# Performance work log

Measured on AMD Instinct MI355X. Metric: run time of the kernel, lower is better.

The kernel has to match this reference:

```python
import jax, jax.numpy as jnp
import numpy as np

NUM_HIDDENS = 512
NUM_HEADS = 4
B, S = 4, 2048


def setup_inputs() -> dict:
    key = jax.random.key(0)
    ks = jax.random.split(key, 10)
    H = NUM_HIDDENS
    scale = 1.0 / np.sqrt(H)
    return {
        "queries": jax.random.normal(ks[0], (B, S, H), jnp.float32),
        "keys": jax.random.normal(ks[1], (B, S, H), jnp.float32),
        "values": jax.random.normal(ks[2], (B, S, H), jnp.float32),
        "attention_mask": jax.random.randint(ks[3], (B, S), 0, 2).astype(bool),
        "Wq": jax.random.normal(ks[4], (H, H), jnp.float32) * scale,
        "bq": jnp.zeros((H,), jnp.float32),
        "Wk": jax.random.normal(ks[5], (H, H), jnp.float32) * scale,
        "bk": jnp.zeros((H,), jnp.float32),
        "Wv": jax.random.normal(ks[6], (H, H), jnp.float32) * scale,
        "bv": jnp.zeros((H,), jnp.float32),
    }


def reference(queries, keys, values, attention_mask, Wq, bq, Wk, bk, Wv, bv):
    B_, S_, H = queries.shape
    nh = NUM_HEADS
    dh = H // nh

    # QKV projections with ReLU (as in the original Sequential(Linear, ReLU))
    q = jax.nn.relu(jnp.einsum("bsh,oh->bso", queries, Wq) + bq)
    k = jax.nn.relu(jnp.einsum("bsh,oh->bso", keys, Wk) + bk)
    v = jax.nn.relu(jnp.einsum("bsh,oh->bso", values, Wv) + bv)

    # chunk along last dim + stack dim=1  ==  reshape [B,S,nh,dh] -> [B,nh,S,dh]
    qs = q.reshape(B_, S_, nh, dh).transpose(0, 2, 1, 3)
    ks_ = k.reshape(B_, S_, nh, dh).transpose(0, 2, 1, 3)
    vs = v.reshape(B_, S_, nh, dh).transpose(0, 2, 1, 3)

    # scores [B, nh, S, S]
    score = jnp.einsum("bhqd,bhkd->bhqk", qs, ks_) / jnp.sqrt(jnp.float32(dh))

    # 'enc' mask: [B,S] -> [B,1,S,1], fills entire QUERY rows (faithful quirk)
    row_mask = attention_mask[:, None, :, None]
    score = jnp.where(row_mask, jnp.float32(-1e9), score)

    attn = jax.nn.softmax(score, axis=-1)
    a = jnp.einsum("bhqk,bhkd->bhqd", attn, vs)  # [B, nh, S, dh]

    # faithful quirk: permute(0,1,3,2) then reshape to (B, S, H)
    a = jnp.transpose(a, (0, 1, 3, 2)).reshape(B_, S_, H)
    return a + queries
```

## Files before the change

### kernel.cpp

```cpp
#include <hip/hip_runtime.h>
#include <hip/hip_bf16.h>

typedef __attribute__((ext_vector_type(8)))  __bf16 bf16x8;
typedef __attribute__((ext_vector_type(4)))  __bf16 bf16x4;
typedef __attribute__((ext_vector_type(2)))  __bf16 bf16x2;
typedef __attribute__((ext_vector_type(4)))  float  f32x4;
typedef __attribute__((ext_vector_type(16))) float  f32x16;

#define MFMA16(a,b,c) __builtin_amdgcn_mfma_f32_16x16x32_bf16((a),(b),(c),0,0,0)
#define MFMA32(a,b,c) __builtin_amdgcn_mfma_f32_32x32x16_bf16((a),(b),(c),0,0,0)

__device__ inline void gload_lds16(const __bf16* g, __bf16* l) {
  __builtin_amdgcn_global_load_lds(
      (const __attribute__((address_space(1))) void*)g,
      (__attribute__((address_space(3))) void*)l, 16, 0, 0);
}

__global__ __launch_bounds__(256) void proj_kernel(
    const float* __restrict__ Xq, const float* __restrict__ Xk,
    const float* __restrict__ Xv, const float* __restrict__ Wq,
    const float* __restrict__ Wk, const float* __restrict__ Wv,
    const float* __restrict__ bq, const float* __restrict__ bk,
    const float* __restrict__ bv, __bf16* __restrict__ dq,
    __bf16* __restrict__ dk, __bf16* __restrict__ dv)
{
  const int which = blockIdx.z;
  const float* X   = which == 0 ? Xq : which == 1 ? Xk : Xv;
  const float* W   = which == 0 ? Wq : which == 1 ? Wk : Wv;
  const float* bias= which == 0 ? bq : which == 1 ? bk : bv;
  __bf16* dst      = which == 0 ? dq : which == 1 ? dk : dv;
  const float oscale = which == 0 ? 0.12751744710339033f : 1.0f;
  const int mode = (which == 2);

  __shared__ __bf16 Al[64][72];
  __shared__ __bf16 Wl[64][72];
  const int tid  = threadIdx.x;
  const int lane = tid & 63;
  const int w    = tid >> 6;
  const int wr = w >> 1, wc = w & 1;
  const int mbase = blockIdx.x * 64;
  const int nbase = blockIdx.y * 64;
  const int arow = lane & 15;
  const int kgrp = (lane >> 4) * 8;
  f32x4 acc[2][2] = {};

  for (int k0 = 0; k0 < 512; k0 += 64) {
    __syncthreads();
#pragma unroll
    for (int i = 0; i < 4; ++i) {
      int idx = tid + i * 256;
      int r = idx >> 4, c = (idx & 15) * 4;
      float4 a  = *(const float4*)&X[(size_t)(mbase + r) * 512 + k0 + c];
      float4 bb = *(const float4*)&W[(size_t)(nbase + r) * 512 + k0 + c];
      bf16x4 av, bv2;
      av[0] = (__bf16)a.x;  av[1] = (__bf16)a.y;  av[2] = (__bf16)a.z;  av[3] = (__bf16)a.w;
      bv2[0] = (__bf16)bb.x; bv2[1] = (__bf16)bb.y; bv2[2] = (__bf16)bb.z; bv2[3] = (__bf16)bb.w;
      *(bf16x4*)&Al[r][c] = av;
      *(bf16x4*)&Wl[r][c] = bv2;
    }
    __syncthreads();
#pragma unroll
    for (int kk = 0; kk < 2; ++kk) {
      bf16x8 af[2], bfr[2];
      const int kcol = kk * 32 + kgrp;
#pragma unroll
      for (int m = 0; m < 2; ++m)
        af[m] = *(bf16x8*)&Al[wr * 32 + m * 16 + arow][kcol];
#pragma unroll
      for (int n = 0; n < 2; ++n)
        bfr[n] = *(bf16x8*)&Wl[wc * 32 + n * 16 + arow][kcol];
#pragma unroll
      for (int m = 0; m < 2; ++m)
#pragma unroll
        for (int n = 0; n < 2; ++n)
          acc[m][n] = MFMA16(af[m], bfr[n], acc[m][n]);
    }
  }

#pragma unroll
  for (int m = 0; m < 2; ++m) {
#pragma unroll
    for (int n = 0; n < 2; ++n) {
      int col  = nbase + wc * 32 + n * 16 + (lane & 15);
      int row0 = mbase + wr * 32 + m * 16 + ((lane >> 4) << 2);
      float bsv = bias[col];
      int h = col >> 7, d = col & 127;
#pragma unroll
      for (int r = 0; r < 4; ++r) {
        float v = acc[m][n][r] + bsv;
        v = (v > 0.0f ? v : 0.0f) * oscale;
        int mm = row0 + r;
        int b = mm >> 11, s = mm & 2047;
        if (mode == 0)
          dst[((size_t)(b * 4 + h) * 2048 + s) * 128 + d] = (__bf16)v;
        else
          dst[((size_t)(b * 4 + h) * 128 + d) * 2048 + s] = (__bf16)v;
      }
    }
  }
}

__global__ __launch_bounds__(256, 2) void attn_kernel(
    const __bf16* __restrict__ qh, const __bf16* __restrict__ kh,
    const __bf16* __restrict__ vt, const int* __restrict__ mask,
    const float* __restrict__ queries, float* __restrict__ out)
{
  __shared__ __align__(16) __bf16 Kl[2][64 * 128];
  __shared__ __align__(16) __bf16 Vl[2][128 * 64];

  const int tid  = threadIdx.x;
  const int lane = tid & 63;
  const int w    = tid >> 6;
  const int qw   = w & 1;
  const int kw   = w >> 1;
  const int r5   = lane & 31;
  const int hi32 = lane >> 5;

  const int blk = blockIdx.x;
  const int xcd = blk & 7;
  const int idx = blk >> 3;
  const int bh  = xcd * 2 + (idx & 1);
  const int qt  = idx >> 1;
  const int b = bh >> 2, h = bh & 3;
  const int qbase = qt * 64 + qw * 32;

  const __bf16* qptr = qh + (size_t)bh * 2048 * 128;
  const __bf16* kptr = kh + (size_t)bh * 2048 * 128;
  const __bf16* vptr = vt + (size_t)bh * 128 * 2048;

  bf16x8 qf[8];
#pragma unroll
  for (int ds = 0; ds < 8; ++ds)
    qf[ds] = *(const bf16x8*)&qptr[(size_t)(qbase + r5) * 128 + ds * 16 + hi32 * 8];

  const bool mrow = mask[b * 2048 + qbase + r5] != 0;

  float m_st = -1e30f, l_st = 0.f;
  f32x16 oacc[4] = {};

  auto stageK = [&](int buf, int kv0) {
#pragma unroll
    for (int i = 0; i < 4; ++i) {
      int ob = i * 4096 + w * 1024;
      int o  = ob + lane * 16;
      int r  = o >> 8;
      int s  = ((o >> 4) & 15) ^ (r & 7);
      gload_lds16(kptr + (size_t)(kv0 + r) * 128 + s * 8, &Kl[buf][ob >> 1]);
    }
  };
  auto stageV = [&](int buf, int kv0) {
#pragma unroll
    for (int i = 0; i < 4; ++i) {
      int ob = i * 4096 + w * 1024;
      int o  = ob + lane * 16;
      int r  = o >> 7;
      int s  = ((o >> 4) & 7) ^ (r & 7);
      gload_lds16(vptr + (size_t)r * 2048 + kv0 + s * 8, &Vl[buf][ob >> 1]);
    }
  };

  stageK(0, 0);
  stageV(0, 0);

  for (int t = 0; t < 32; ++t) {
    const int cur = t & 1;
    if (t < 31) {
      stageK(cur ^ 1, (t + 1) * 64);
      stageV(cur ^ 1, (t + 1) * 64);
      asm volatile("s_waitcnt vmcnt(8)" ::: "memory");
    } else {
      asm volatile("s_waitcnt vmcnt(0)" ::: "memory");
    }
    __builtin_amdgcn_s_barrier();

    f32x16 sacc = {};
    __builtin_amdgcn_s_setprio(1);
#pragma unroll
    for (int ds = 0; ds < 8; ++ds) {
      int row = kw * 32 + r5;
      int sl  = ((ds * 2 + hi32) ^ (row & 7)) * 8;
      bf16x8 kf = *(bf16x8*)&Kl[cur][row * 128 + sl];
      sacc = MFMA32(kf, qf[ds], sacc);
    }
    __builtin_amdgcn_s_setprio(0);

#pragma unroll
    for (int r = 0; r < 16; ++r)
      sacc[r] = mrow ? -1e9f : sacc[r];

    float pmax = sacc[0];
#pragma unroll
    for (int r = 1; r < 16; ++r) pmax = fmaxf(pmax, sacc[r]);
    pmax = fmaxf(pmax, __shfl_xor(pmax, 32));

    if (!__all(pmax - m_st <= 8.0f)) {
      float mn = fmaxf(m_st, pmax);
      float rs = __builtin_amdgcn_exp2f(m_st - mn);
      m_st = mn;
      l_st *= rs;
#pragma unroll
      for (int dblk = 0; dblk < 4; ++dblk)
#pragma unroll
        for (int r = 0; r < 16; ++r)
          oacc[dblk][r] *= rs;
    }

    float rsum = 0.f;
#pragma unroll
    for (int r = 0; r < 16; ++r) {
      float p = __builtin_amdgcn_exp2f(sacc[r] - m_st);
      sacc[r] = p;
      rsum += p;
    }
    rsum += __shfl_xor(rsum, 32);
    l_st += rsum;

    unsigned pk[8];
#pragma unroll
    for (int g = 0; g < 8; ++g) {
      bf16x2 tp;
      tp[0] = (__bf16)sacc[2 * g];
      tp[1] = (__bf16)sacc[2 * g + 1];
      pk[g] = __builtin_bit_cast(unsigned, tp);
    }
    bf16x8 pf[2];
#pragma unroll
    for (int s = 0; s < 2; ++s) {
      unsigned a0 = pk[4 * s + 0], a1 = pk[4 * s + 1];
      unsigned b0 = pk[4 * s + 2], b1 = pk[4 * s + 3];
      asm("v_permlane32_swap_b32 %0, %1" : "+v"(a0), "+v"(b0));
      asm("v_permlane32_swap_b32 %0, %1" : "+v"(a1), "+v"(b1));
      union { unsigned u[4]; bf16x8 v; } pu;
      pu.u[0] = a0; pu.u[1] = a1; pu.u[2] = b0; pu.u[3] = b1;
      pf[s] = pu.v;
    }

    __builtin_amdgcn_s_setprio(1);
#pragma unroll
    for (int dblk = 0; dblk < 4; ++dblk) {
#pragma unroll
      for (int s = 0; s < 2; ++s) {
        int row = dblk * 32 + r5;
        int s0  = kw * 4 + s * 2 + hi32;
        int sl  = (s0 ^ (row & 7)) * 8;
        bf16x8 vf = *(bf16x8*)&Vl[cur][row * 64 + sl];
        oacc[dblk] = MFMA32(vf, pf[s], oacc[dblk]);
      }
    }
    __builtin_amdgcn_s_setprio(0);

    __builtin_amdgcn_s_barrier();
  }

  __syncthreads();
  float* Ml = (float*)&Kl[0][0];
  float* Ll = Ml + 64;
  float* Ob = Ml + 128;

  if (kw == 1) {
    if (hi32 == 0) { Ml[qw * 32 + r5] = m_st; Ll[qw * 32 + r5] = l_st; }
    float* dst = Ob + (size_t)(qw * 64 + lane) * 68;
#pragma unroll
    for (int dblk = 0; dblk < 4; ++dblk)
      *(f32x16*)(dst + dblk * 16) = oacc[dblk];
  }
  __syncthreads();

  if (kw == 0) {
    float m1 = Ml[qw * 32 + r5], l1 = Ll[qw * 32 + r5];
    float mm = fmaxf(m_st, m1);
    float w0 = __builtin_amdgcn_exp2f(m_st - mm);
    float w1 = __builtin_amdgcn_exp2f(m1 - mm);
    float inv = 1.0f / (l_st * w0 + l1 * w1);
    const float* src = Ob + (size_t)(qw * 64 + lane) * 68;

    const int qhi = qt >> 3;
    const int col = (qt & 7) * 64 + qw * 32 + r5;
#pragma unroll
    for (int dblk = 0; dblk < 4; ++dblk) {
      f32x16 o1 = *(const f32x16*)(src + dblk * 16);
#pragma unroll
      for (int r = 0; r < 16; ++r) {
        int d = dblk * 32 + (r & 3) + 8 * (r >> 2) + 4 * hi32;
        int srow = h * 512 + d * 4 + qhi;
        size_t o = ((size_t)b * 2048 + srow) * 512 + col;
        out[o] = (oacc[dblk][r] * w0 + o1[r] * w1) * inv + queries[o];
      }
    }
  }
}

extern "C" void kernel_launch(void* const* d_in, const int* in_sizes, int n_in,
                              void* d_out, int out_size, void* d_ws, size_t ws_size,
                              hipStream_t stream) {
  const float* queries = (const float*)d_in[0];
  const float* keys    = (const float*)d_in[1];
  const float* values  = (const float*)d_in[2];
  const int*   mask    = (const int*)d_in[3];
  const float* Wq = (const float*)d_in[4];
  const float* bq = (const float*)d_in[5];
  const float* Wk = (const float*)d_in[6];
  const float* bk = (const float*)d_in[7];
  const float* Wv = (const float*)d_in[8];
  const float* bv = (const float*)d_in[9];
  float* out = (float*)d_out;

  const size_t per = (size_t)4 * 4 * 2048 * 128;
  __bf16* qhp = (__bf16*)d_ws;
  __bf16* khp = qhp + per;
  __bf16* vtp = khp + per;

  dim3 pb(256), pg(128, 8, 3);
  proj_kernel<<<pg, pb, 0, stream>>>(queries, keys, values, Wq, Wk, Wv,
                                     bq, bk, bv, qhp, khp, vtp);

  attn_kernel<<<dim3(512), dim3(256), 0, stream>>>(qhp, khp, vtp, mask, queries, out);
}
```

Baseline: 99.29 us.

## Split projection into bf16 convert pass and double-buffered async-LDS GEMM

Adds a separate kernel that converts the fp32 inputs and weights to bf16 in workspace. The projection GEMM is rewritten with 128x128 tiles, XOR-swizzled LDS, and double-buffered global_load_lds staging, so the next k-tile loads while MFMAs run on the current one. This removes the synchronous fp32 load, convert, and store to LDS in the GEMM loop and raises reuse per tile. In exchange it adds an extra kernel launch and a full extra read and write of the inputs through global memory, and the larger tiles mean fewer blocks (768 versus 3072).

Result: faster. 94.46 us (-4.9%).

```diff
diff --git a/kernel.cpp b/kernel.cpp
--- a/kernel.cpp
+++ b/kernel.cpp
@@ -16,75 +16,129 @@
       (__attribute__((address_space(3))) void*)l, 16, 0, 0);
 }
 
-__global__ __launch_bounds__(256) void proj_kernel(
+__global__ __launch_bounds__(256) void convert_kernel(
     const float* __restrict__ Xq, const float* __restrict__ Xk,
     const float* __restrict__ Xv, const float* __restrict__ Wq,
     const float* __restrict__ Wk, const float* __restrict__ Wv,
+    __bf16* __restrict__ dXq, __bf16* __restrict__ dXk, __bf16* __restrict__ dXv,
+    __bf16* __restrict__ dWq, __bf16* __restrict__ dWk, __bf16* __restrict__ dWv)
+{
+  const int which = blockIdx.y;
+  const float* src;
+  __bf16* dst;
+  size_t idx;
+  if (blockIdx.x < 4096) {
+    src = which == 0 ? Xq : which == 1 ? Xk : Xv;
+    dst = which == 0 ? dXq : which == 1 ? dXk : dXv;
+    idx = (size_t)blockIdx.x * 256 + threadIdx.x;
+  } else {
+    src = which == 0 ? Wq : which == 1 ? Wk : Wv;
+    dst = which == 0 ? dWq : which == 1 ? dWk : dWv;
+    idx = (size_t)(blockIdx.x - 4096) * 256 + threadIdx.x;
+  }
+  float4 v = *(const float4*)&src[idx * 4];
+  bf16x4 o;
+  o[0] = (__bf16)v.x; o[1] = (__bf16)v.y; o[2] = (__bf16)v.z; o[3] = (__bf16)v.w;
+  *(bf16x4*)&dst[idx * 4] = o;
+}
+
+__global__ __launch_bounds__(256, 2) void gemm_kernel(
+    const __bf16* __restrict__ Xqb, const __bf16* __restrict__ Xkb,
+    const __bf16* __restrict__ Xvb, const __bf16* __restrict__ Wqb,
+    const __bf16* __restrict__ Wkb, const __bf16* __restrict__ Wvb,
     const float* __restrict__ bq, const float* __restrict__ bk,
     const float* __restrict__ bv, __bf16* __restrict__ dq,
     __bf16* __restrict__ dk, __bf16* __restrict__ dv)
 {
   const int which = blockIdx.z;
-  const float* X   = which == 0 ? Xq : which == 1 ? Xk : Xv;
-  const float* W   = which == 0 ? Wq : which == 1 ? Wk : Wv;
-  const float* bias= which == 0 ? bq : which == 1 ? bk : bv;
-  __bf16* dst      = which == 0 ? dq : which == 1 ? dk : dv;
+  const __bf16* X   = which == 0 ? Xqb : which == 1 ? Xkb : Xvb;
+  const __bf16* W   = which == 0 ? Wqb : which == 1 ? Wkb : Wvb;
+  const float* bias = which == 0 ? bq : which == 1 ? bk : bv;
+  __bf16* dst       = which == 0 ? dq : which == 1 ? dk : dv;
   const float oscale = which == 0 ? 0.12751744710339033f : 1.0f;
   const int mode = (which == 2);
 
-  __shared__ __bf16 Al[64][72];
-  __shared__ __bf16 Wl[64][72];
+  __shared__ __align__(16) __bf16 Al[2][128 * 64];
+  __shared__ __align__(16) __bf16 Bl[2][128 * 64];
+
   const int tid  = threadIdx.x;
   const int lane = tid & 63;
   const int w    = tid >> 6;
   const int wr = w >> 1, wc = w & 1;
-  const int mbase = blockIdx.x * 64;
-  const int nbase = blockIdx.y * 64;
+  const int mbase = blockIdx.x * 128;
+  const int nbase = blockIdx.y * 128;
   const int arow = lane & 15;
-  const int kgrp = (lane >> 4) * 8;
-  f32x4 acc[2][2] = {};
-
-  for (int k0 = 0; k0 < 512; k0 += 64) {
-    __syncthreads();
+  const int hi   = lane >> 4;
+  const int kgrp = hi * 8;
+
+  f32x4 acc[4][4] = {};
+
+  auto stage = [&](int buf, int k0) {
 #pragma unroll
     for (int i = 0; i < 4; ++i) {
-      int idx = tid + i * 256;
-      int r = idx >> 4, c = (idx & 15) * 4;
-      float4 a  = *(const float4*)&X[(size_t)(mbase + r) * 512 + k0 + c];
-      float4 bb = *(const float4*)&W[(size_t)(nbase + r) * 512 + k0 + c];
-      bf16x4 av, bv2;
-      av[0] = (__bf16)a.x;  av[1] = (__bf16)a.y;  av[2] = (__bf16)a.z;  av[3] = (__bf16)a.w;
-      bv2[0] = (__bf16)bb.x; bv2[1] = (__bf16)bb.y; bv2[2] = (__bf16)bb.z; bv2[3] = (__bf16)bb.w;
-      *(bf16x4*)&Al[r][c] = av;
-      *(bf16x4*)&Wl[r][c] = bv2;
-    }
-    __syncthreads();
+      int ob = w * 4096 + i * 1024;
+      int o  = ob + lane * 16;
+      int r  = o >> 7;
+      int s  = ((o >> 4) & 7) ^ (r & 7);
+      gload_lds16(X + (size_t)(mbase + r) * 512 + k0 + s * 8, &Al[buf][ob >> 1]);
+    }
+#pragma unroll
+    for (int i = 0; i < 4; ++i) {
+      int ob = w * 4096 + i * 1024;
+      int o  = ob + lane * 16;
+      int r  = o >> 7;
+      int s  = ((o >> 4) & 7) ^ (r & 7);
+      gload_lds16(W + (size_t)(nbase + r) * 512 + k0 + s * 8, &Bl[buf][ob >> 1]);
+    }
+  };
+
+  stage(0, 0);
+
+  for (int t = 0; t < 8; ++t) {
+    const int cur = t & 1;
+    if (t < 7) {
+      stage(cur ^ 1, (t + 1) * 64);
+      asm volatile("s_waitcnt vmcnt(8)" ::: "memory");
+    } else {
+      asm volatile("s_waitcnt vmcnt(0)" ::: "memory");
+    }
+    __builtin_amdgcn_s_barrier();
+
+    __builtin_amdgcn_s_setprio(1);
 #pragma unroll
     for (int kk = 0; kk < 2; ++kk) {
-      bf16x8 af[2], bfr[2];
-      const int kcol = kk * 32 + kgrp;
-#pragma unroll
-      for (int m = 0; m < 2; ++m)
-        af[m] = *(bf16x8*)&Al[wr * 32 + m * 16 + arow][kcol];
-#pragma unroll
-      for (int n = 0; n < 2; ++n)
-        bfr[n] = *(bf16x8*)&Wl[wc * 32 + n * 16 + arow][kcol];
-#pragma unroll
-      for (int m = 0; m < 2; ++m)
-#pragma unroll
-        for (int n = 0; n < 2; ++n)
+      bf16x8 af[4], bfr[4];
+#pragma unroll
+      for (int m = 0; m < 4; ++m) {
+        int row = wr * 64 + m * 16 + arow;
+        int sl  = ((kk * 4 + hi) ^ (row & 7)) * 8;
+        af[m] = *(bf16x8*)&Al[cur][row * 64 + sl];
+      }
+#pragma unroll
+      for (int n = 0; n < 4; ++n) {
+        int row = wc * 64 + n * 16 + arow;
+        int sl  = ((kk * 4 + hi) ^ (row & 7)) * 8;
+        bfr[n] = *(bf16x8*)&Bl[cur][row * 64 + sl];
+      }
+#pragma unroll
+      for (int m = 0; m < 4; ++m)
+#pragma unroll
+        for (int n = 0; n < 4; ++n)
           acc[m][n] = MFMA16(af[m], bfr[n], acc[m][n]);
     }
-  }
-
-#pragma unroll
-  for (int m = 0; m < 2; ++m) {
-#pragma unroll
-    for (int n = 0; n < 2; ++n) {
-      int col  = nbase + wc * 32 + n * 16 + (lane & 15);
-      int row0 = mbase + wr * 32 + m * 16 + ((lane >> 4) << 2);
-      float bsv = bias[col];
-      int h = col >> 7, d = col & 127;
+    __builtin_amdgcn_s_setprio(0);
+
+    __builtin_amdgcn_s_barrier();
+  }
+
+#pragma unroll
+  for (int n = 0; n < 4; ++n) {
+    int col = nbase + wc * 64 + n * 16 + arow;
+    float bsv = bias[col];
+    int h = col >> 7, d = col & 127;
+#pragma unroll
+    for (int m = 0; m < 4; ++m) {
+      int row0 = mbase + wr * 64 + m * 16 + hi * 4;
 #pragma unroll
       for (int r = 0; r < 4; ++r) {
         float v = acc[m][n][r] + bsv;
@@ -305,14 +359,23 @@
   const float* bv = (const float*)d_in[9];
   float* out = (float*)d_out;
 
-  const size_t per = (size_t)4 * 4 * 2048 * 128;
+  const size_t perX = (size_t)8192 * 512;
+  const size_t perW = (size_t)512 * 512;
   __bf16* qhp = (__bf16*)d_ws;
-  __bf16* khp = qhp + per;
-  __bf16* vtp = khp + per;
-
-  dim3 pb(256), pg(128, 8, 3);
-  proj_kernel<<<pg, pb, 0, stream>>>(queries, keys, values, Wq, Wk, Wv,
-                                     bq, bk, bv, qhp, khp, vtp);
+  __bf16* khp = qhp + perX;
+  __bf16* vtp = khp + perX;
+  __bf16* Xqb = vtp + perX;
+  __bf16* Xkb = Xqb + perX;
+  __bf16* Xvb = Xkb + perX;
+  __bf16* Wqb = Xvb + perX;
+  __bf16* Wkb = Wqb + perW;
+  __bf16* Wvb = Wkb + perW;
+
+  convert_kernel<<<dim3(4352, 3), dim3(256), 0, stream>>>(
+      queries, keys, values, Wq, Wk, Wv, Xqb, Xkb, Xvb, Wqb, Wkb, Wvb);
+
+  gemm_kernel<<<dim3(64, 4, 3), dim3(256), 0, stream>>>(
+      Xqb, Xkb, Xvb, Wqb, Wkb, Wvb, bq, bk, bv, qhp, khp, vtp);
 
   attn_kernel<<<dim3(512), dim3(256), 0, stream>>>(qhp, khp, vtp, mask, queries, out);
 }
```
